# Kernel tuning notes

Measured on AMD Instinct MI355X. Metric: run time of the kernel, lower is better.

The kernel has to match this reference:

```python
import jax, jax.numpy as jnp
import numpy as np
from jax import lax

WINDOW_SIZE = 5
GRAD_THRESH = 0.15
MAX_ITER = 5
EPS = 1e-8


def setup_inputs() -> dict:
    key = jax.random.key(0)
    k1, k2, k3 = jax.random.split(key, 3)
    B, M, T = 16, 128, 12000
    return {
        "mel_features": jax.random.normal(k1, (B, M, T), jnp.float32),
        "spectral_features": jax.random.normal(k2, (B, T), jnp.float32),
        "initial_boundaries": jax.random.uniform(k3, (B, T), dtype=jnp.float32),
        "similarity_weights": jnp.ones(3, jnp.float32) / 3.0,
    }


def _consistency_scores(mel, spec, weights):
    # mel: (B, M, T), spec: (B, T), weights: (3,)
    B, M, T = mel.shape
    # cosine similarity between consecutive frames (vectorized over t)
    a, b = mel[:, :, :-1], mel[:, :, 1:]
    dot = jnp.sum(a * b, axis=1)
    na = jnp.sqrt(jnp.sum(a * a, axis=1))
    nb = jnp.sqrt(jnp.sum(b * b, axis=1))
    cos = dot / (jnp.maximum(na, EPS) * jnp.maximum(nb, EPS))  # (B, T-1)
    mel_sim = jnp.pad(cos, ((0, 0), (1, 0)))  # t=0 stays 0 (torch init zeros)

    spec_diff = jnp.abs(spec[:, 1:] - spec[:, :-1])
    spec_sim = jnp.pad(1.0 / (1.0 + spec_diff), ((0, 0), (1, 0)), constant_values=1.0)

    # avg_pool1d(mean over mel bins, k, stride=1, pad=k//2, count_include_pad)
    k = min(WINDOW_SIZE, T)
    mean_mel = jnp.mean(mel, axis=1)  # (B, T)
    pad = k // 2
    padded = jnp.pad(mean_mel, ((0, 0), (pad, pad)))
    cs = jnp.pad(jnp.cumsum(padded, axis=1), ((0, 0), (1, 0)))
    smooth = (cs[:, k:] - cs[:, :-k]) / k  # (B, T)
    # torch.std default is unbiased (ddof=1)
    temporal = 1.0 - jnp.std(smooth, axis=1, ddof=1, keepdims=True)  # (B, 1)
    temporal = jnp.broadcast_to(temporal, (B, T))

    return weights[0] * mel_sim + weights[1] * spec_sim + weights[2] * temporal


def _adjustments(candidates, cons):
    # local mean of cons over [t-2, t+3) clipped to [0, T)
    B, T = cons.shape
    cs = jnp.pad(jnp.cumsum(cons, axis=1), ((0, 0), (1, 0)))  # (B, T+1)
    t = jnp.arange(T)
    lo = jnp.maximum(t - 2, 0)
    hi = jnp.minimum(t + 3, T)
    local = (cs[:, hi] - cs[:, lo]) / (hi - lo).astype(cons.dtype)
    interior = (t >= 1) & (t <= T - 2)  # loop ran over range(1, T-1)
    active = (candidates > 0.5) & interior
    return jnp.where(active & (local > 0.7), -0.1,
                     jnp.where(active & (local < 0.4), 0.1, 0.0)).astype(cons.dtype)


def reference(mel_features, spectral_features, initial_boundaries, similarity_weights):
    weights = jax.nn.softmax(similarity_weights)
    cons = _consistency_scores(mel_features, spectral_features, weights)
    # gradient-based candidates are fixed across iterations (cons is fixed)
    grads = jnp.pad(jnp.abs(cons[:, 1:] - cons[:, :-1]), ((0, 0), (1, 0)))
    cand_static = (grads > GRAD_THRESH).astype(cons.dtype)

    def body(carry, _):
        refined, done = carry
        candidates = jnp.maximum(cand_static, refined)
        adj = _adjustments(candidates, cons)
        adj = jnp.where(done, 0.0, adj)  # replicate early break by freezing
        new_refined = jnp.clip(refined + adj, 0.0, 1.0)
        new_done = done | (jnp.sum(jnp.abs(adj)) < 0.01)
        return (new_refined, new_done), None

    (refined, _), _ = lax.scan(body, (initial_boundaries, jnp.array(False)),
                               None, length=MAX_ITER)
    return refined
```

## Files before the change

kernel.cpp:

```cpp
#include <hip/hip_runtime.h>
#include <cstdint>

#define BB 16
#define MM 128
#define TT 12000
constexpr int BT = BB * TT;

#define CH_SB 28
#define CH_F4 1792
#define CH_BYTES 28672
#define NCHUNK 27

__global__ void k1_colstats(const float* __restrict__ mel,
                            float* __restrict__ ssq,
                            float* __restrict__ dotv,
                            float* __restrict__ cmean,
                            unsigned int* __restrict__ counts) {
    if (blockIdx.x == 0 && blockIdx.y == 0 && threadIdx.x < 8)
        counts[threadIdx.x] = 0u;
    const int b = blockIdx.y;
    const int t = blockIdx.x * blockDim.x + threadIdx.x;
    if (t >= TT) return;
    const float* base = mel + (size_t)b * MM * TT;
    float accd = 0.f, accq = 0.f, accs = 0.f;
    {
#pragma clang fp contract(off)
        for (int m = 0; m < MM; ++m) {
            const float* rowp = base + (size_t)m * TT;
            float cur = rowp[t];
            float prev = (t > 0) ? rowp[t - 1] : 0.f;
            accd += prev * cur;
            accq += cur * cur;
            accs += cur;
        }
    }
    size_t i = (size_t)b * TT + t;
    ssq[i] = accq; dotv[i] = accd; cmean[i] = accs * (1.0f / MM);
}

__global__ void kA_temporal(const float* __restrict__ cmean,
                            float* __restrict__ temporal) {
    const int b = blockIdx.x;
    const int tid = threadIdx.x;
    __shared__ __align__(16) float row_s[TT];
    __shared__ float red[256];
    __shared__ float mean_s;
    const float4* c4 = (const float4*)(cmean + (size_t)b * TT);
    float4* r4 = (float4*)row_s;
    for (int i = tid; i < TT / 4; i += 256) r4[i] = c4[i];
    __syncthreads();

    float s = 0.f;
    for (int t = tid; t < TT; t += 256) {
        float v = 0.f;
        int lo = t - 2 < 0 ? 0 : t - 2;
        int hi = t + 2 >= TT ? TT - 1 : t + 2;
        for (int j = lo; j <= hi; ++j) v += row_s[j];
        s += v / 5.0f;
    }
    red[tid] = s; __syncthreads();
    for (int o = 128; o > 0; o >>= 1) {
        if (tid < o) red[tid] += red[tid + o];
        __syncthreads();
    }
    if (tid == 0) mean_s = red[0] / (float)TT;
    __syncthreads();
    float mean = mean_s;
    float ss = 0.f;
    for (int t = tid; t < TT; t += 256) {
        float v = 0.f;
        int lo = t - 2 < 0 ? 0 : t - 2;
        int hi = t + 2 >= TT ? TT - 1 : t + 2;
        for (int j = lo; j <= hi; ++j) v += row_s[j];
        float sm = v / 5.0f - mean;
        ss += sm * sm;
    }
    red[tid] = ss; __syncthreads();
    for (int o = 128; o > 0; o >>= 1) {
        if (tid < o) red[tid] += red[tid + o];
        __syncthreads();
    }
    if (tid == 0) {
        float var = red[0] / (float)(TT - 1);
        temporal[b] = 1.0f - sqrtf(var);
    }
}

__global__ void kB_cons(const float* __restrict__ ssq,
                        const float* __restrict__ dotv,
                        const float* __restrict__ spec,
                        const float* __restrict__ temporal,
                        const float* __restrict__ wraw,
                        float* __restrict__ cons,
                        float* __restrict__ consq) {
    const int idx = blockIdx.x * 256 + threadIdx.x;
    const int b = idx / TT;
    const int t = idx - b * TT;
    float x0 = wraw[0], x1 = wraw[1], x2 = wraw[2];
    float mx = fmaxf(x0, fmaxf(x1, x2));
    float e0 = expf(x0 - mx), e1 = expf(x1 - mx), e2 = expf(x2 - mx);
    float es = (e0 + e1) + e2;
    float w0 = e0 / es, w1 = e1 / es, w2 = e2 / es;
    float mel_sim, spec_sim;
    if (t == 0) { mel_sim = 0.f; spec_sim = 1.f; }
    else {
        float na = fmaxf(sqrtf(ssq[idx - 1]), 1e-8f);
        float nb = fmaxf(sqrtf(ssq[idx]),     1e-8f);
        float den = na * nb; asm volatile("" : "+v"(den));
        mel_sim = dotv[idx] / den;
        float d = fabsf(spec[idx] - spec[idx - 1]);
        spec_sim = 1.0f / (1.0f + d);
    }
    float pa = w0 * mel_sim;     asm volatile("" : "+v"(pa));
    float pb = w1 * spec_sim;    asm volatile("" : "+v"(pb));
    float pc = w2 * temporal[b]; asm volatile("" : "+v"(pc));
    float c = (pa + pb) + pc;
    cons[idx] = c;
    consq[((t >> 2) * 16 + b) * 4 + (t & 3)] = c;
}

#define SB16(a0,a1,a2,a3, b0,b1,b2,b3, c0,c1,c2,c3, d0,d1,d2,d3, S0,S1,S2,S3, P0,P1,P2,P3) \
    "s_waitcnt lgkmcnt(12)\n\t" \
    "v_add_f32 v" a0 ", %0, v" a0 "\n\t" \
    "v_add_f32 v" a1 ", v" a0 ", v" a1 "\n\t" \
    "v_add_f32 v" a2 ", v" a1 ", v" a2 "\n\t" \
    "v_add_f32 v" a3 ", v" a2 ", v" a3 "\n\t" \
    "v_add_f32 v" b0 ", v" a3 ", v" b0 "\n\t" \
    "v_add_f32 v" b1 ", v" b0 ", v" b1 "\n\t" \
    "v_add_f32 v" b2 ", v" b1 ", v" b2 "\n\t" \
    "v_add_f32 v" b3 ", v" b2 ", v" b3 "\n\t" \
    "v_add_f32 v" c0 ", v" b3 ", v" c0 "\n\t" \
    "v_add_f32 v" c1 ", v" c0 ", v" c1 "\n\t" \
    "v_add_f32 v" c2 ", v" c1 ", v" c2 "\n\t" \
    "v_add_f32 v" c3 ", v" c2 ", v" c3 "\n\t" \
    "v_add_f32 v" d0 ", v" c3 ", v" d0 "\n\t" \
    "v_add_f32 v" d1 ", v" d0 ", v" d1 "\n\t" \
    "v_add_f32 v" d2 ", v" d1 ", v" d2 "\n\t" \
    "v_add_f32 v" d3 ", v" d2 ", v" d3 "\n\t" \
    "v_mov_b32 %0, v" d3 "\n\t" \
    "global_store_dwordx4 v40, v[" a0 ":" a3 "], %1 offset:" S0 "\n\t" \
    "global_store_dwordx4 v40, v[" b0 ":" b3 "], %1 offset:" S1 "\n\t" \
    "global_store_dwordx4 v40, v[" c0 ":" c3 "], %1 offset:" S2 "\n\t" \
    "global_store_dwordx4 v40, v[" d0 ":" d3 "], %1 offset:" S3 "\n\t" \
    "ds_read_b128 v[" a0 ":" a3 "], v41 offset:" P0 "\n\t" \
    "ds_read_b128 v[" b0 ":" b3 "], v41 offset:" P1 "\n\t" \
    "ds_read_b128 v[" c0 ":" c3 "], v41 offset:" P2 "\n\t" \
    "ds_read_b128 v[" d0 ":" d3 "], v41 offset:" P3 "\n\t"

__global__ void __launch_bounds__(256)
kC_scan16(const float* __restrict__ consq,
          float* __restrict__ CSq) {
    const int tid = threadIdx.x;
    __shared__ __align__(16) float bufA[CH_F4 * 4];
    __shared__ __align__(16) float bufB[CH_F4 * 4];
    float4* bA4 = (float4*)bufA;
    float4* bB4 = (float4*)bufB;
    const float4* src4 = (const float4*)consq;

    for (int i = tid; i < CH_F4; i += 256) bA4[i] = src4[i];
    __syncthreads();

    float carry = 0.f;
    for (int c = 0; c < NCHUNK; ++c) {
        if (tid >= 64 && c + 1 < NCHUNK) {
            const float4* s4 = src4 + (size_t)(c + 1) * CH_F4;
            float4* d4 = ((c + 1) & 1) ? bB4 : bA4;
            for (int i = tid - 64; i < CH_F4; i += 192) d4[i] = s4[i];
        }
        if (tid < BB) {
            uint32_t lds_addr = (uint32_t)(uintptr_t)((c & 1) ? bufB : bufA)
                              + (uint32_t)(tid * 16);
            uint32_t goff = (uint32_t)(c * CH_BYTES + tid * 16);
            asm volatile(
                "v_mov_b32 v40, %3\n\t"
                "v_mov_b32 v41, %2\n\t"
                "ds_read_b128 v[48:51],   v41 offset:0\n\t"
                "ds_read_b128 v[52:55],   v41 offset:256\n\t"
                "ds_read_b128 v[56:59],   v41 offset:512\n\t"
                "ds_read_b128 v[60:63],   v41 offset:768\n\t"
                "ds_read_b128 v[64:67],   v41 offset:1024\n\t"
                "ds_read_b128 v[68:71],   v41 offset:1280\n\t"
                "ds_read_b128 v[72:75],   v41 offset:1536\n\t"
                "ds_read_b128 v[76:79],   v41 offset:1792\n\t"
                "ds_read_b128 v[80:83],   v41 offset:2048\n\t"
                "ds_read_b128 v[84:87],   v41 offset:2304\n\t"
                "ds_read_b128 v[88:91],   v41 offset:2560\n\t"
                "ds_read_b128 v[92:95],   v41 offset:2816\n\t"
                "ds_read_b128 v[96:99],   v41 offset:3072\n\t"
                "ds_read_b128 v[100:103], v41 offset:3328\n\t"
                "ds_read_b128 v[104:107], v41 offset:3584\n\t"
                "ds_read_b128 v[108:111], v41 offset:3840\n\t"
                "s_mov_b32 s20, 7\n\t"
                "3:\n\t"
                SB16("48","49","50","51", "52","53","54","55",
                     "56","57","58","59", "60","61","62","63",
                     "0","256","512","768", "4096","4352","4608","4864")
                SB16("64","65","66","67", "68","69","70","71",
                     "72","73","74","75", "76","77","78","79",
                     "1024","1280","1536","1792", "5120","5376","5632","5888")
                SB16("80","81","82","83", "84","85","86","87",
                     "88","89","90","91", "92","93","94","95",
                     "2048","2304","2560","2816", "6144","6400","6656","6912")
                SB16("96","97","98","99", "100","101","102","103",
                     "104","105","106","107", "108","109","110","111",
                     "3072","3328","3584","3840", "7168","7424","7680","7936")
                "v_add_u32 v40, 0x1000, v40\n\t"
                "v_add_u32 v41, 0x1000, v41\n\t"
                "s_sub_u32 s20, s20, 1\n\t"
                "s_cmp_lg_u32 s20, 0\n\t"
                "s_cbranch_scc1 3b\n\t"
                "s_waitcnt vmcnt(0) lgkmcnt(0)\n\t"
                : "+v"(carry)
                : "s"(CSq), "v"(lds_addr), "v"(goff)
                : "v40", "v41",
                  "v48", "v49", "v50", "v51", "v52", "v53", "v54", "v55",
                  "v56", "v57", "v58", "v59", "v60", "v61", "v62", "v63",
                  "v64", "v65", "v66", "v67", "v68", "v69", "v70", "v71",
                  "v72", "v73", "v74", "v75", "v76", "v77", "v78", "v79",
                  "v80", "v81", "v82", "v83", "v84", "v85", "v86", "v87",
                  "v88", "v89", "v90", "v91", "v92", "v93", "v94", "v95",
                  "v96", "v97", "v98", "v99", "v100", "v101", "v102", "v103",
                  "v104", "v105", "v106", "v107", "v108", "v109", "v110", "v111",
                  "s20", "scc", "memory");
        }
        __syncthreads();
    }
}

__global__ void kD_prepare(const float* __restrict__ cons,
                           const float* __restrict__ CSq,
                           const float* __restrict__ init,
                           float* __restrict__ stepv,
                           float* __restrict__ candf,
                           unsigned int* __restrict__ counts) {
    const int idx = blockIdx.x * 256 + threadIdx.x;
    const int b = idx / TT;
    const int t = idx - b * TT;
    __shared__ unsigned sflag[5];
    if (threadIdx.x < 5) sflag[threadIdx.x] = 0u;
    __syncthreads();

    int lo = t - 2; if (lo < 0) lo = 0;
    int hi = t + 3; if (hi > TT) hi = TT;
    int uh = hi - 1;
    float csH = CSq[((uh >> 2) * 16 + b) * 4 + (uh & 3)];
    float csL = 0.f;
    if (lo > 0) {
        int ul = lo - 1;
        csL = CSq[((ul >> 2) * 16 + b) * 4 + (ul & 3)];
    }
    float local = (csH - csL) / (float)(hi - lo);
    float dir = (local > 0.7f) ? -0.1f : ((local < 0.4f) ? 0.1f : 0.0f);
    bool interior = (t >= 1) && (t <= TT - 2);
    float step = interior ? dir : 0.0f;
    float g = (t == 0) ? 0.f : fabsf(cons[idx] - cons[idx - 1]);
    float cand = (g > 0.15f) ? 1.f : 0.f;
    float r = init[idx];
    bool nz[5];
#pragma unroll
    for (int j = 0; j < 5; ++j) {
        float adj = (fmaxf(cand, r) > 0.5f) ? step : 0.0f;
        nz[j] = (adj != 0.0f);
        r = fminf(fmaxf(r + adj, 0.0f), 1.0f);
    }
    stepv[idx] = step; candf[idx] = cand;
    const int lane = threadIdx.x & 63;
#pragma unroll
    for (int j = 0; j < 5; ++j) {
        unsigned long long mb = __ballot(nz[j]);
        if (lane == 0 && mb) atomicOr(&sflag[j], 1u);
    }
    __syncthreads();
    if (threadIdx.x < 5 && sflag[threadIdx.x]) counts[threadIdx.x] = 1u;
}

__global__ void k_final(const float* __restrict__ init,
                        const float* __restrict__ stepv,
                        const float* __restrict__ candf,
                        const unsigned int* __restrict__ counts,
                        float* __restrict__ outp) {
    const int idx = blockIdx.x * 256 + threadIdx.x;
    float r = init[idx];
    float step = stepv[idx];
    float cand = candf[idx];
    unsigned c[5];
#pragma unroll
    for (int j = 0; j < 5; ++j) c[j] = counts[j];
#pragma unroll
    for (int j = 0; j < 5; ++j) {
        if (c[j] == 0u) break;
        float adj = (fmaxf(cand, r) > 0.5f) ? step : 0.0f;
        r = fminf(fmaxf(r + adj, 0.0f), 1.0f);
    }
    outp[idx] = r;
}

extern "C" void kernel_launch(void* const* d_in, const int* in_sizes, int n_in,
                              void* d_out, int out_size, void* d_ws, size_t ws_size,
                              hipStream_t stream) {
    const float* mel  = (const float*)d_in[0];
    const float* spec = (const float*)d_in[1];
    const float* init = (const float*)d_in[2];
    const float* wts  = (const float*)d_in[3];

    float* ws = (float*)d_ws;
    float* ssq   = ws;
    float* dotv  = ws + 192000;
    float* cmean = ws + 384000;
    float* cons  = ws + 576000;
    float* consq = ws + 768000;
    float* CSq   = ws + 964608;
    float* stepv = ws + 1161216;
    float* candf = ws + 1353216;
    float* temporal = ws + 1545216;
    unsigned int* counts = (unsigned int*)(ws + 1545232);

    dim3 g1((TT + 255) / 256, BB);
    k1_colstats<<<g1, 256, 0, stream>>>(mel, ssq, dotv, cmean, counts);
    kA_temporal<<<BB, 256, 0, stream>>>(cmean, temporal);
    kB_cons<<<BT / 256, 256, 0, stream>>>(ssq, dotv, spec, temporal, wts, cons, consq);
    kC_scan16<<<1, 256, 0, stream>>>(consq, CSq);
    kD_prepare<<<BT / 256, 256, 0, stream>>>(cons, CSq, init, stepv, candf, counts);
    k_final<<<BT / 256, 256, 0, stream>>>(init, stepv, candf, counts, (float*)d_out);
}
```

Before: 139.1 us.

## Invert scan pipeline: scan threads load global directly, helper warps store results

The single-block serial prefix scan is restructured. Scan lanes now issue global loads straight into a 192-register ring, several chunks ahead, and write their running sums to a double-buffered LDS staging area. Helper warps then copy the staged results to global memory after each barrier. This is meant to take global load latency and store issue off the serial add chain, at the cost of very high VGPR use, hand-counted vmcnt waits, and a resized workspace layout.

```diff
diff --git a/kernel.cpp b/kernel.cpp
--- a/kernel.cpp
+++ b/kernel.cpp
@@ -6,10 +6,6 @@
 #define TT 12000
 constexpr int BT = BB * TT;
 
-#define CH_SB 28
-#define CH_F4 1792
-#define CH_BYTES 28672
-#define NCHUNK 27
 
 __global__ void k1_colstats(const float* __restrict__ mel,
                             float* __restrict__ ssq,
@@ -119,9 +115,9 @@
     consq[((t >> 2) * 16 + b) * 4 + (t & 3)] = c;
 }
 
-#define SB16(a0,a1,a2,a3, b0,b1,b2,b3, c0,c1,c2,c3, d0,d1,d2,d3, S0,S1,S2,S3, P0,P1,P2,P3) \
-    "s_waitcnt lgkmcnt(12)\n\t" \
-    "v_add_f32 v" a0 ", %0, v" a0 "\n\t" \
+#define SBX(a0,a1,a2,a3, b0,b1,b2,b3, c0,c1,c2,c3, d0,d1,d2,d3) \
+    "s_waitcnt vmcnt(44)\n\t" \
+    "v_add_f32 v" a0 ", v43, v" a0 "\n\t" \
     "v_add_f32 v" a1 ", v" a0 ", v" a1 "\n\t" \
     "v_add_f32 v" a2 ", v" a1 ", v" a2 "\n\t" \
     "v_add_f32 v" a3 ", v" a2 ", v" a3 "\n\t" \
@@ -137,93 +133,109 @@
     "v_add_f32 v" d1 ", v" d0 ", v" d1 "\n\t" \
     "v_add_f32 v" d2 ", v" d1 ", v" d2 "\n\t" \
     "v_add_f32 v" d3 ", v" d2 ", v" d3 "\n\t" \
-    "v_mov_b32 %0, v" d3 "\n\t" \
-    "global_store_dwordx4 v40, v[" a0 ":" a3 "], %1 offset:" S0 "\n\t" \
-    "global_store_dwordx4 v40, v[" b0 ":" b3 "], %1 offset:" S1 "\n\t" \
-    "global_store_dwordx4 v40, v[" c0 ":" c3 "], %1 offset:" S2 "\n\t" \
-    "global_store_dwordx4 v40, v[" d0 ":" d3 "], %1 offset:" S3 "\n\t" \
-    "ds_read_b128 v[" a0 ":" a3 "], v41 offset:" P0 "\n\t" \
-    "ds_read_b128 v[" b0 ":" b3 "], v41 offset:" P1 "\n\t" \
-    "ds_read_b128 v[" c0 ":" c3 "], v41 offset:" P2 "\n\t" \
-    "ds_read_b128 v[" d0 ":" d3 "], v41 offset:" P3 "\n\t"
+    "v_mov_b32 v43, v" d3 "\n\t" \
+    "ds_write_b128 v44, v[" a0 ":" a3 "] offset:0\n\t" \
+    "ds_write_b128 v44, v[" b0 ":" b3 "] offset:256\n\t" \
+    "ds_write_b128 v44, v[" c0 ":" c3 "] offset:512\n\t" \
+    "ds_write_b128 v44, v[" d0 ":" d3 "] offset:768\n\t" \
+    "global_load_dwordx4 v[" a0 ":" a3 "], v40, %0 offset:0\n\t" \
+    "global_load_dwordx4 v[" b0 ":" b3 "], v40, %0 offset:256\n\t" \
+    "global_load_dwordx4 v[" c0 ":" c3 "], v40, %0 offset:512\n\t" \
+    "global_load_dwordx4 v[" d0 ":" d3 "], v40, %0 offset:768\n\t" \
+    "v_add_u32 v44, 0x400, v44\n\t" \
+    "v_add_u32 v40, 0x400, v40\n\t"
+
+#define PRO(a0,a1,a2,a3, b0,b1,b2,b3, c0,c1,c2,c3, d0,d1,d2,d3) \
+    "global_load_dwordx4 v[" a0 ":" a3 "], v40, %0 offset:0\n\t" \
+    "global_load_dwordx4 v[" b0 ":" b3 "], v40, %0 offset:256\n\t" \
+    "global_load_dwordx4 v[" c0 ":" c3 "], v40, %0 offset:512\n\t" \
+    "global_load_dwordx4 v[" d0 ":" d3 "], v40, %0 offset:768\n\t" \
+    "v_add_u32 v40, 0x400, v40\n\t"
+
+#define R0  "48","49","50","51","52","53","54","55","56","57","58","59","60","61","62","63"
+#define R1  "64","65","66","67","68","69","70","71","72","73","74","75","76","77","78","79"
+#define R2  "80","81","82","83","84","85","86","87","88","89","90","91","92","93","94","95"
+#define R3  "96","97","98","99","100","101","102","103","104","105","106","107","108","109","110","111"
+#define R4  "112","113","114","115","116","117","118","119","120","121","122","123","124","125","126","127"
+#define R5  "128","129","130","131","132","133","134","135","136","137","138","139","140","141","142","143"
+#define R6  "144","145","146","147","148","149","150","151","152","153","154","155","156","157","158","159"
+#define R7  "160","161","162","163","164","165","166","167","168","169","170","171","172","173","174","175"
+#define R8  "176","177","178","179","180","181","182","183","184","185","186","187","188","189","190","191"
+#define R9  "192","193","194","195","196","197","198","199","200","201","202","203","204","205","206","207"
+#define R10 "208","209","210","211","212","213","214","215","216","217","218","219","220","221","222","223"
+#define R11 "224","225","226","227","228","229","230","231","232","233","234","235","236","237","238","239"
+#define XP(M, ...) M(__VA_ARGS__)
+
+#define CHUNK12 \
+    XP(SBX, R0)  XP(SBX, R1)  XP(SBX, R2)  XP(SBX, R3) \
+    XP(SBX, R4)  XP(SBX, R5)  XP(SBX, R6)  XP(SBX, R7) \
+    XP(SBX, R8)  XP(SBX, R9)  XP(SBX, R10) XP(SBX, R11) \
+    "s_waitcnt lgkmcnt(0)\n\t" \
+    "s_barrier\n\t"
 
 __global__ void __launch_bounds__(256)
 kC_scan16(const float* __restrict__ consq,
           float* __restrict__ CSq) {
     const int tid = threadIdx.x;
-    __shared__ __align__(16) float bufA[CH_F4 * 4];
-    __shared__ __align__(16) float bufB[CH_F4 * 4];
-    float4* bA4 = (float4*)bufA;
-    float4* bB4 = (float4*)bufB;
-    const float4* src4 = (const float4*)consq;
-
-    for (int i = tid; i < CH_F4; i += 256) bA4[i] = src4[i];
-    __syncthreads();
-
-    float carry = 0.f;
-    for (int c = 0; c < NCHUNK; ++c) {
-        if (tid >= 64 && c + 1 < NCHUNK) {
-            const float4* s4 = src4 + (size_t)(c + 1) * CH_F4;
-            float4* d4 = ((c + 1) & 1) ? bB4 : bA4;
-            for (int i = tid - 64; i < CH_F4; i += 192) d4[i] = s4[i];
+    __shared__ __align__(16) float lbuf[6144];
+
+    if (tid < BB) {
+        uint32_t goff  = (uint32_t)(tid * 16);
+        uint32_t laddr = (uint32_t)(uintptr_t)&lbuf[0] + (uint32_t)(tid * 16);
+        asm volatile(
+            "v_mov_b32 v40, %1\n\t"
+            "v_mov_b32 v44, %2\n\t"
+            "v_mov_b32 v43, 0\n\t"
+            XP(PRO, R0)  XP(PRO, R1)  XP(PRO, R2)  XP(PRO, R3)
+            XP(PRO, R4)  XP(PRO, R5)  XP(PRO, R6)  XP(PRO, R7)
+            XP(PRO, R8)  XP(PRO, R9)  XP(PRO, R10) XP(PRO, R11)
+            "s_mov_b32 s20, 32\n\t"
+            "3:\n\t"
+            CHUNK12
+            CHUNK12
+            "v_add_u32 v44, 0xffffa000, v44\n\t"
+            "s_sub_u32 s20, s20, 1\n\t"
+            "s_cmp_lg_u32 s20, 0\n\t"
+            "s_cbranch_scc1 3b\n\t"
+            "s_waitcnt vmcnt(0) lgkmcnt(0)\n\t"
+            :
+            : "s"(consq), "v"(goff), "v"(laddr)
+            : "v40", "v43", "v44",
+              "v48","v49","v50","v51","v52","v53","v54","v55",
+              "v56","v57","v58","v59","v60","v61","v62","v63",
+              "v64","v65","v66","v67","v68","v69","v70","v71",
+              "v72","v73","v74","v75","v76","v77","v78","v79",
+              "v80","v81","v82","v83","v84","v85","v86","v87",
+              "v88","v89","v90","v91","v92","v93","v94","v95",
+              "v96","v97","v98","v99","v100","v101","v102","v103",
+              "v104","v105","v106","v107","v108","v109","v110","v111",
+              "v112","v113","v114","v115","v116","v117","v118","v119",
+              "v120","v121","v122","v123","v124","v125","v126","v127",
+              "v128","v129","v130","v131","v132","v133","v134","v135",
+              "v136","v137","v138","v139","v140","v141","v142","v143",
+              "v144","v145","v146","v147","v148","v149","v150","v151",
+              "v152","v153","v154","v155","v156","v157","v158","v159",
+              "v160","v161","v162","v163","v164","v165","v166","v167",
+              "v168","v169","v170","v171","v172","v173","v174","v175",
+              "v176","v177","v178","v179","v180","v181","v182","v183",
+              "v184","v185","v186","v187","v188","v189","v190","v191",
+              "v192","v193","v194","v195","v196","v197","v198","v199",
+              "v200","v201","v202","v203","v204","v205","v206","v207",
+              "v208","v209","v210","v211","v212","v213","v214","v215",
+              "v216","v217","v218","v219","v220","v221","v222","v223",
+              "v224","v225","v226","v227","v228","v229","v230","v231",
+              "v232","v233","v234","v235","v236","v237","v238","v239",
+              "s20", "scc", "memory");
+    }
+    if (tid >= 64) {
+        float4* dst4 = (float4*)CSq;
+        const float4* b4 = (const float4*)lbuf;
+        for (int c = 0; c < 64; ++c) {
+            asm volatile("s_barrier" ::: "memory");
+            const float4* s4 = b4 + (size_t)(c & 1) * 768;
+            float4* d4 = dst4 + (size_t)c * 768;
+            for (int i = tid - 64; i < 768; i += 192) d4[i] = s4[i];
         }
-        if (tid < BB) {
-            uint32_t lds_addr = (uint32_t)(uintptr_t)((c & 1) ? bufB : bufA)
-                              + (uint32_t)(tid * 16);
-            uint32_t goff = (uint32_t)(c * CH_BYTES + tid * 16);
-            asm volatile(
-                "v_mov_b32 v40, %3\n\t"
-                "v_mov_b32 v41, %2\n\t"
-                "ds_read_b128 v[48:51],   v41 offset:0\n\t"
-                "ds_read_b128 v[52:55],   v41 offset:256\n\t"
-                "ds_read_b128 v[56:59],   v41 offset:512\n\t"
-                "ds_read_b128 v[60:63],   v41 offset:768\n\t"
-                "ds_read_b128 v[64:67],   v41 offset:1024\n\t"
-                "ds_read_b128 v[68:71],   v41 offset:1280\n\t"
-                "ds_read_b128 v[72:75],   v41 offset:1536\n\t"
-                "ds_read_b128 v[76:79],   v41 offset:1792\n\t"
-                "ds_read_b128 v[80:83],   v41 offset:2048\n\t"
-                "ds_read_b128 v[84:87],   v41 offset:2304\n\t"
-                "ds_read_b128 v[88:91],   v41 offset:2560\n\t"
-                "ds_read_b128 v[92:95],   v41 offset:2816\n\t"
-                "ds_read_b128 v[96:99],   v41 offset:3072\n\t"
-                "ds_read_b128 v[100:103], v41 offset:3328\n\t"
-                "ds_read_b128 v[104:107], v41 offset:3584\n\t"
-                "ds_read_b128 v[108:111], v41 offset:3840\n\t"
-                "s_mov_b32 s20, 7\n\t"
-                "3:\n\t"
-                SB16("48","49","50","51", "52","53","54","55",
-                     "56","57","58","59", "60","61","62","63",
-                     "0","256","512","768", "4096","4352","4608","4864")
-                SB16("64","65","66","67", "68","69","70","71",
-                     "72","73","74","75", "76","77","78","79",
-                     "1024","1280","1536","1792", "5120","5376","5632","5888")
-                SB16("80","81","82","83", "84","85","86","87",
-                     "88","89","90","91", "92","93","94","95",
-                     "2048","2304","2560","2816", "6144","6400","6656","6912")
-                SB16("96","97","98","99", "100","101","102","103",
-                     "104","105","106","107", "108","109","110","111",
-                     "3072","3328","3584","3840", "7168","7424","7680","7936")
-                "v_add_u32 v40, 0x1000, v40\n\t"
-                "v_add_u32 v41, 0x1000, v41\n\t"
-                "s_sub_u32 s20, s20, 1\n\t"
-                "s_cmp_lg_u32 s20, 0\n\t"
-                "s_cbranch_scc1 3b\n\t"
-                "s_waitcnt vmcnt(0) lgkmcnt(0)\n\t"
-                : "+v"(carry)
-                : "s"(CSq), "v"(lds_addr), "v"(goff)
-                : "v40", "v41",
-                  "v48", "v49", "v50", "v51", "v52", "v53", "v54", "v55",
-                  "v56", "v57", "v58", "v59", "v60", "v61", "v62", "v63",
-                  "v64", "v65", "v66", "v67", "v68", "v69", "v70", "v71",
-                  "v72", "v73", "v74", "v75", "v76", "v77", "v78", "v79",
-                  "v80", "v81", "v82", "v83", "v84", "v85", "v86", "v87",
-                  "v88", "v89", "v90", "v91", "v92", "v93", "v94", "v95",
-                  "v96", "v97", "v98", "v99", "v100", "v101", "v102", "v103",
-                  "v104", "v105", "v106", "v107", "v108", "v109", "v110", "v111",
-                  "s20", "scc", "memory");
-        }
-        __syncthreads();
     }
 }
 
@@ -309,11 +321,11 @@
     float* cmean = ws + 384000;
     float* cons  = ws + 576000;
     float* consq = ws + 768000;
-    float* CSq   = ws + 964608;
-    float* stepv = ws + 1161216;
-    float* candf = ws + 1353216;
-    float* temporal = ws + 1545216;
-    unsigned int* counts = (unsigned int*)(ws + 1545232);
+    float* CSq   = ws + 967680;
+    float* stepv = ws + 1164288;
+    float* candf = ws + 1356288;
+    float* temporal = ws + 1548288;
+    unsigned int* counts = (unsigned int*)(ws + 1548304);
 
     dim3 g1((TT + 255) / 256, BB);
     k1_colstats<<<g1, 256, 0, stream>>>(mel, ssq, dotv, cmean, counts);
```

Result: faster. 135.5 us (-2.6%).

## Recompute step/candidate in final kernel and rechunk single-block scan

Applied to the files above, without the earlier changes.

The prepare kernel no longer writes step and candidate arrays. The final kernel recomputes them from cons and the prefix sums, which trades two stores plus two loads per element for some extra arithmetic and gathers. The serial scan kernel now uses 32 chunks of 1536 float4 instead of 27, and its prefetch uses unrolled register-staged loads. The vmcnt wait moves out of the per-chunk asm block to a single wait after the loop, so global stores can overlap across chunks. This relies on the prefetch and LDS layout staying correct for the new chunk size.

```diff
diff --git a/kernel.cpp b/kernel.cpp
--- a/kernel.cpp
+++ b/kernel.cpp
@@ -6,10 +6,6 @@
 #define TT 12000
 constexpr int BT = BB * TT;
 
-#define CH_SB 28
-#define CH_F4 1792
-#define CH_BYTES 28672
-#define NCHUNK 27
 
 __global__ void k1_colstats(const float* __restrict__ mel,
                             float* __restrict__ ssq,
@@ -151,26 +147,29 @@
 kC_scan16(const float* __restrict__ consq,
           float* __restrict__ CSq) {
     const int tid = threadIdx.x;
-    __shared__ __align__(16) float bufA[CH_F4 * 4];
-    __shared__ __align__(16) float bufB[CH_F4 * 4];
-    float4* bA4 = (float4*)bufA;
-    float4* bB4 = (float4*)bufB;
+    __shared__ __align__(16) float lbuf[2 * 6144 + 1024];
+    float4* b4 = (float4*)lbuf;
     const float4* src4 = (const float4*)consq;
 
-    for (int i = tid; i < CH_F4; i += 256) bA4[i] = src4[i];
+    for (int i = tid; i < 1536; i += 256) b4[i] = src4[i];
     __syncthreads();
 
     float carry = 0.f;
-    for (int c = 0; c < NCHUNK; ++c) {
-        if (tid >= 64 && c + 1 < NCHUNK) {
-            const float4* s4 = src4 + (size_t)(c + 1) * CH_F4;
-            float4* d4 = ((c + 1) & 1) ? bB4 : bA4;
-            for (int i = tid - 64; i < CH_F4; i += 192) d4[i] = s4[i];
+    for (int c = 0; c < 32; ++c) {
+        if (tid >= 64 && c + 1 < 32) {
+            const float4* s4 = src4 + (size_t)(c + 1) * 1536;
+            float4* d4 = b4 + (size_t)((c + 1) & 1) * 1536;
+            const int lane = tid - 64;
+            float4 tmp[8];
+#pragma unroll
+            for (int i = 0; i < 8; ++i) tmp[i] = s4[lane + 192 * i];
+#pragma unroll
+            for (int i = 0; i < 8; ++i) d4[lane + 192 * i] = tmp[i];
         }
         if (tid < BB) {
-            uint32_t lds_addr = (uint32_t)(uintptr_t)((c & 1) ? bufB : bufA)
-                              + (uint32_t)(tid * 16);
-            uint32_t goff = (uint32_t)(c * CH_BYTES + tid * 16);
+            uint32_t laddr = (uint32_t)(uintptr_t)(lbuf + (size_t)(c & 1) * 6144)
+                           + (uint32_t)(tid * 16);
+            uint32_t goff = (uint32_t)(c * 24576 + tid * 16);
             asm volatile(
                 "v_mov_b32 v40, %3\n\t"
                 "v_mov_b32 v41, %2\n\t"
@@ -190,7 +189,7 @@
                 "ds_read_b128 v[100:103], v41 offset:3328\n\t"
                 "ds_read_b128 v[104:107], v41 offset:3584\n\t"
                 "ds_read_b128 v[108:111], v41 offset:3840\n\t"
-                "s_mov_b32 s20, 7\n\t"
+                "s_mov_b32 s20, 6\n\t"
                 "3:\n\t"
                 SB16("48","49","50","51", "52","53","54","55",
                      "56","57","58","59", "60","61","62","63",
@@ -209,9 +208,9 @@
                 "s_sub_u32 s20, s20, 1\n\t"
                 "s_cmp_lg_u32 s20, 0\n\t"
                 "s_cbranch_scc1 3b\n\t"
-                "s_waitcnt vmcnt(0) lgkmcnt(0)\n\t"
+                "s_waitcnt lgkmcnt(0)\n\t"
                 : "+v"(carry)
-                : "s"(CSq), "v"(lds_addr), "v"(goff)
+                : "s"(CSq), "v"(laddr), "v"(goff)
                 : "v40", "v41",
                   "v48", "v49", "v50", "v51", "v52", "v53", "v54", "v55",
                   "v56", "v57", "v58", "v59", "v60", "v61", "v62", "v63",
@@ -225,14 +224,13 @@
         }
         __syncthreads();
     }
-}
-
-__global__ void kD_prepare(const float* __restrict__ cons,
-                           const float* __restrict__ CSq,
-                           const float* __restrict__ init,
-                           float* __restrict__ stepv,
-                           float* __restrict__ candf,
-                           unsigned int* __restrict__ counts) {
+    if (tid < BB) asm volatile("s_waitcnt vmcnt(0)" ::: "memory");
+}
+
+__global__ void kD_flags(const float* __restrict__ cons,
+                         const float* __restrict__ CSq,
+                         const float* __restrict__ init,
+                         unsigned int* __restrict__ counts) {
     const int idx = blockIdx.x * 256 + threadIdx.x;
     const int b = idx / TT;
     const int t = idx - b * TT;
@@ -263,7 +261,6 @@
         nz[j] = (adj != 0.0f);
         r = fminf(fmaxf(r + adj, 0.0f), 1.0f);
     }
-    stepv[idx] = step; candf[idx] = cand;
     const int lane = threadIdx.x & 63;
 #pragma unroll
     for (int j = 0; j < 5; ++j) {
@@ -274,15 +271,32 @@
     if (threadIdx.x < 5 && sflag[threadIdx.x]) counts[threadIdx.x] = 1u;
 }
 
-__global__ void k_final(const float* __restrict__ init,
-                        const float* __restrict__ stepv,
-                        const float* __restrict__ candf,
+__global__ void k_final(const float* __restrict__ cons,
+                        const float* __restrict__ CSq,
+                        const float* __restrict__ init,
                         const unsigned int* __restrict__ counts,
                         float* __restrict__ outp) {
     const int idx = blockIdx.x * 256 + threadIdx.x;
+    const int b = idx / TT;
+    const int t = idx - b * TT;
+
+    int lo = t - 2; if (lo < 0) lo = 0;
+    int hi = t + 3; if (hi > TT) hi = TT;
+    int uh = hi - 1;
+    float csH = CSq[((uh >> 2) * 16 + b) * 4 + (uh & 3)];
+    float csL = 0.f;
+    if (lo > 0) {
+        int ul = lo - 1;
+        csL = CSq[((ul >> 2) * 16 + b) * 4 + (ul & 3)];
+    }
+    float local = (csH - csL) / (float)(hi - lo);
+    float dir = (local > 0.7f) ? -0.1f : ((local < 0.4f) ? 0.1f : 0.0f);
+    bool interior = (t >= 1) && (t <= TT - 2);
+    float step = interior ? dir : 0.0f;
+    float g = (t == 0) ? 0.f : fabsf(cons[idx] - cons[idx - 1]);
+    float cand = (g > 0.15f) ? 1.f : 0.f;
+
     float r = init[idx];
-    float step = stepv[idx];
-    float cand = candf[idx];
     unsigned c[5];
 #pragma unroll
     for (int j = 0; j < 5; ++j) c[j] = counts[j];
@@ -310,16 +324,14 @@
     float* cons  = ws + 576000;
     float* consq = ws + 768000;
     float* CSq   = ws + 964608;
-    float* stepv = ws + 1161216;
-    float* candf = ws + 1353216;
-    float* temporal = ws + 1545216;
-    unsigned int* counts = (unsigned int*)(ws + 1545232);
+    float* temporal = ws + 1161216;
+    unsigned int* counts = (unsigned int*)(ws + 1161232);
 
     dim3 g1((TT + 255) / 256, BB);
     k1_colstats<<<g1, 256, 0, stream>>>(mel, ssq, dotv, cmean, counts);
     kA_temporal<<<BB, 256, 0, stream>>>(cmean, temporal);
     kB_cons<<<BT / 256, 256, 0, stream>>>(ssq, dotv, spec, temporal, wts, cons, consq);
     kC_scan16<<<1, 256, 0, stream>>>(consq, CSq);
-    kD_prepare<<<BT / 256, 256, 0, stream>>>(cons, CSq, init, stepv, candf, counts);
-    k_final<<<BT / 256, 256, 0, stream>>>(init, stepv, candf, counts, (float*)d_out);
-}
+    kD_flags<<<BT / 256, 256, 0, stream>>>(cons, CSq, init, counts);
+    k_final<<<BT / 256, 256, 0, stream>>>(cons, CSq, init, counts, (float*)d_out);
+}
```

After: 128.2 us. -7.9%, faster.
